# Kernel tuning notes

Hardware: AMD Instinct MI355X
Metric: run time of the kernel (lower is better)

## Reference

```python
import math
import jax, jax.numpy as jnp
import numpy as np

B, L, D, H, DFF, T, V = 512, 128, 128, 4, 256, 2048, 20000
LN_EPS = 1e-5
LOG_SIGMA0 = math.log(0.1)


def _keygen(base):
    c = [0]
    def nk():
        k = jax.random.fold_in(base, c[0]); c[0] += 1
        return k
    return nk


def bayes_linear(x, wmu, wls, bmu, bls, nk):
    # weight = mu + exp(log_sigma) * eps (fresh eps every call, as in BayesLinear.forward)
    w = wmu + jnp.exp(wls) * jax.random.normal(nk(), wmu.shape, wmu.dtype)
    b = bmu + jnp.exp(bls) * jax.random.normal(nk(), bmu.shape, bmu.dtype)
    return jnp.einsum('...d,od->...o', x, w) + b


def layer_norm(x, g, b):
    m = x.mean(-1, keepdims=True)
    v = ((x - m) ** 2).mean(-1, keepdims=True)
    return (x - m) / jnp.sqrt(v + LN_EPS) * g + b


def mha(q, k, v, wmu, wls, bmu, bls, nk):
    # wmu: [4, D, D] for q, k, v, o projections
    dk = D // H
    def proj(x, i):
        return bayes_linear(x, wmu[i], wls[i], bmu[i], bls[i], nk)
    def split(x):
        return x.reshape(B, L, H, dk).transpose(0, 2, 1, 3)
    Q, K, Vh = split(proj(q, 0)), split(proj(k, 1)), split(proj(v, 2))
    probs = jax.nn.softmax(jnp.einsum('bhqd,bhkd->bhqk', Q, K) / math.sqrt(dk), axis=-1)
    out = jnp.einsum('bhqk,bhkd->bhqd', probs, Vh).transpose(0, 2, 1, 3).reshape(B, L, D)
    return bayes_linear(out, wmu[3], wls[3], bmu[3], bls[3], nk)


def setup_inputs() -> dict:
    key = jax.random.key(0)
    ks = iter(jax.random.split(key, 64))
    def u(shape, fan_in):
        s = 1.0 / math.sqrt(fan_in)
        return jax.random.uniform(next(ks), shape, jnp.float32, -s, s)
    def ls(shape):
        return jnp.full(shape, LOG_SIGMA0, jnp.float32)
    return dict(
        event_set=jax.random.randint(next(ks), (B, L), 0, V),
        time=jax.random.uniform(next(ks), (B, L), jnp.float32),
        mask=jax.random.randint(next(ks), (B, L), 0, L),
        set_size=jax.random.randint(next(ks), (B,), 1, L),
        emb=jax.random.normal(next(ks), (V, D), jnp.float32),
        dec_wmu=u((2, 8, D, D), D), dec_wls=ls((2, 8, D, D)),
        dec_bmu=u((2, 8, D), D), dec_bls=ls((2, 8, D)),
        ffn1_wmu=u((2, DFF, D), D), ffn1_wls=ls((2, DFF, D)),
        ffn1_bmu=u((2, DFF), D), ffn1_bls=ls((2, DFF)),
        ffn2_wmu=u((2, D, DFF), DFF), ffn2_wls=ls((2, D, DFF)),
        ffn2_bmu=u((2, D), DFF), ffn2_bls=ls((2, D)),
        ln_g=jnp.ones((2, 3, D), jnp.float32), ln_b=jnp.zeros((2, 3, D), jnp.float32),
        alpha_wmu=u((5, T, D), D), alpha_wls=ls((5, T, D)),
        alpha_bmu=u((5, T), D), alpha_bls=ls((5, T)),
        at_wmu=u((5, 1, D), D), at_wls=ls((5, 1, D)),
        at_bmu=u((5, 1), D), at_bls=ls((5, 1)),
        em_w=u((5, T, D), D), em_b=u((5, T), D),
        es_w=u((5, T, D), D), es_b=u((5, T), D),
        tm_w=u((5, 1, D), D), tm_b=u((5, 1), D),
        ts_w=u((5, 1, D), D), ts_b=u((5, 1), D),
    )


def reference(event_set, time, mask, set_size, emb,
              dec_wmu, dec_wls, dec_bmu, dec_bls,
              ffn1_wmu, ffn1_wls, ffn1_bmu, ffn1_bls,
              ffn2_wmu, ffn2_wls, ffn2_bmu, ffn2_bls,
              ln_g, ln_b, alpha_wmu, alpha_wls, alpha_bmu, alpha_bls,
              at_wmu, at_wls, at_bmu, at_bls,
              em_w, em_b, es_w, es_b, tm_w, tm_b, ts_w, ts_b):
    nk = _keygen(jax.random.key(42))
    x = emb[event_set]                                     # [B, L, D]
    # sinusoidal positional encoding driven by `mask` (integer positions)
    pos = mask.astype(jnp.float32)
    div = jnp.exp(jnp.arange(D, dtype=jnp.float32) * (-math.log(10000.0) / D))
    ang = pos[..., None] * div                             # [B, L, D]
    pos_enc = jnp.where((mask % 2 == 0)[..., None], jnp.sin(ang), jnp.cos(ang))
    inp_x = x + pos_enc
    # two decoder layers: self-attn on x, cross-attn against inp_x (dropout = eval identity)
    for l in range(2):
        a = mha(x, x, x, dec_wmu[l, :4], dec_wls[l, :4], dec_bmu[l, :4], dec_bls[l, :4], nk)
        x = layer_norm(x + a, ln_g[l, 0], ln_b[l, 0])
        a = mha(x, inp_x, inp_x, dec_wmu[l, 4:], dec_wls[l, 4:], dec_bmu[l, 4:], dec_bls[l, 4:], nk)
        x = layer_norm(x + a, ln_g[l, 1], ln_b[l, 1])
        h1 = jax.nn.relu(bayes_linear(x, ffn1_wmu[l], ffn1_wls[l], ffn1_bmu[l], ffn1_bls[l], nk))
        f = bayes_linear(h1, ffn2_wmu[l], ffn2_wls[l], ffn2_bmu[l], ffn2_bls[l], nk)
        x = layer_norm(x + f, ln_g[l, 2], ln_b[l, 2])
    h = x[:, 0, :]                                          # [B, D]
    # 5 Bayesian alpha heads -> softmax over mixture dim (vectorized over k)
    aw = alpha_wmu + jnp.exp(alpha_wls) * jax.random.normal(nk(), alpha_wmu.shape)
    ab = alpha_bmu + jnp.exp(alpha_bls) * jax.random.normal(nk(), alpha_bmu.shape)
    alpha = jax.nn.softmax(jnp.einsum('bd,ktd->btk', h, aw) + ab.T[None], axis=2)   # [B, T, 5]
    atw = at_wmu + jnp.exp(at_wls) * jax.random.normal(nk(), at_wmu.shape)
    atb = at_bmu + jnp.exp(at_bls) * jax.random.normal(nk(), at_bmu.shape)
    alpha_t = jax.nn.softmax(jnp.einsum('bd,kd->bk', h, atw[:, 0]) + atb[:, 0][None], axis=1)  # [B, 5]
    # mixture of 5 reparameterized Gaussian predictors (plain Linears)
    means = jnp.einsum('bd,ktd->bkt', h, em_w) + em_b[None]          # [B, 5, T]
    stds = jnp.exp(jnp.einsum('bd,ktd->bkt', h, es_w) + es_b[None])
    noise_e = jax.random.normal(nk(), (B, 5, T))
    event_pred = jnp.sum(jnp.swapaxes(alpha, 1, 2) * (means + stds * noise_e), axis=1)   # [B, T]
    tmeans = jnp.einsum('bd,kd->bk', h, tm_w[:, 0]) + tm_b[:, 0][None]                   # [B, 5]
    tstds = jnp.exp(jnp.einsum('bd,kd->bk', h, ts_w[:, 0]) + ts_b[:, 0][None])
    noise_t = jax.random.normal(nk(), (B, 5))
    time_pred = jnp.sum(alpha_t * (tmeans + tstds * noise_t), axis=1, keepdims=True)     # [B, 1]
    return event_pred, time_pred
```

## Files before the change

kernel.cpp:

```cpp
#include <hip/hip_runtime.h>
#include <cstdint>
#include <cstddef>


#define NB   512
#define NL   128
#define ND   128
#define NH   4
#define NDFF 256
#define NT   2048
#define BL   (NB * NL)

typedef __attribute__((ext_vector_type(8))) short bf16x8;
typedef __attribute__((ext_vector_type(4))) float f32x4;

__host__ __device__ __forceinline__ void tf2x32(uint32_t k0, uint32_t k1,
                                                uint32_t x0, uint32_t x1,
                                                uint32_t& o0, uint32_t& o1)
{
  const uint32_t ks2 = k0 ^ k1 ^ 0x1BD11BDAu;
  x0 += k0; x1 += k1;
#define TF_RND(r) { x0 += x1; x1 = (x1 << (r)) | (x1 >> (32 - (r))); x1 ^= x0; }
  TF_RND(13) TF_RND(15) TF_RND(26) TF_RND(6)
  x0 += k1;  x1 += ks2 + 1u;
  TF_RND(17) TF_RND(29) TF_RND(16) TF_RND(24)
  x0 += ks2; x1 += k0 + 2u;
  TF_RND(13) TF_RND(15) TF_RND(26) TF_RND(6)
  x0 += k0;  x1 += k1 + 3u;
  TF_RND(17) TF_RND(29) TF_RND(16) TF_RND(24)
  x0 += k1;  x1 += ks2 + 4u;
  TF_RND(13) TF_RND(15) TF_RND(26) TF_RND(6)
  x0 += ks2; x1 += k0 + 5u;
#undef TF_RND
  o0 = x0; o1 = x1;
}

__device__ __forceinline__ float erfinv32(float x)
{
  float w = -log1pf(-__fmul_rn(x, x));
  float p;
  if (w < 5.0f) {
    w = w - 2.5f;
    p = 2.81022636e-08f;
    p = __fadd_rn( 3.43273939e-07f, __fmul_rn(p, w));
    p = __fadd_rn(-3.5233877e-06f,  __fmul_rn(p, w));
    p = __fadd_rn(-4.39150654e-06f, __fmul_rn(p, w));
    p = __fadd_rn( 0.00021858087f,  __fmul_rn(p, w));
// ... 106 lines not shown
    int t = i - SA_F2W; int s = t >> 15;
    mu = f2_wmu + t; ls = f2_wls + t;
    c = 18u + 20u * s; idx = (uint32_t)(t & 32767);
    bf_dst = BW_F2 + t;
  } else if (i < SA_AW) {
    int t = i - SA_F2B; int s = t >> 7;
    mu = f2_bmu + t; ls = f2_bls + t;
    c = 19u + 20u * s; idx = (uint32_t)(t & 127);
    f32_dst = BF_F2B + t;
  } else if (i < SA_AB) {
    int t = i - SA_AW;
    mu = a_wmu + t; ls = a_wls + t; c = 40u; idx = (uint32_t)t;
    bf_dst = BW_AW + t;
  } else if (i < SA_ATW) {
    int t = i - SA_AB;
    mu = a_bmu + t; ls = a_bls + t; c = 41u; idx = (uint32_t)t;
    f32_dst = BF_AB + t;
  } else if (i < SA_ATB) {
    int t = i - SA_ATW;
    mu = at_wmu + t; ls = at_wls + t; c = 42u; idx = (uint32_t)t;
    f32_dst = BF_ATW + t;
  } else {
    int t = i - SA_ATB;
    mu = at_bmu + t; ls = at_bls + t; c = 43u; idx = (uint32_t)t;
    f32_dst = BF_ATB + t;
  }
  uint32_t k0, k1;
  tf2x32(0u, 42u, 0u, c, k0, k1);
  float v = mu[0] + expf(ls[0]) * jax_normal_idx(k0, k1, idx);
  if (bf_dst >= 0) wbf[bf_dst] = f2bf(v);
  else             wf32[f32_dst] = v;
}

__global__ __launch_bounds__(256) void embed_pe_kernel(
    const int* __restrict__ ev, const int* __restrict__ mask,
    const float* __restrict__ emb, float* __restrict__ X,
    ushort* __restrict__ Xbf, ushort* __restrict__ INPXbf)
{
  int i = blockIdx.x * 256 + threadIdx.x;
  if (i >= BL * ND) return;
  int d  = i & (ND - 1);
  int bl = i >> 7;
  int e  = ev[bl];
  int mk = mask[bl];
  float x   = emb[(size_t)e * ND + d];
  float div = expf((float)d * (float)(-9.210340371976184 / 128.0));
  float ang = (float)mk * div;
  float pe  = ((mk & 1) == 0) ? sinf(ang) : cosf(ang);
  X[i]      = x;
  Xbf[i]    = f2bf(x);
  INPXbf[i] = f2bf(x + pe);
}

#define STR 136

template<int CROSS>
__global__ __launch_bounds__(512) void attn_block_kernel(
    const ushort* __restrict__ Xbf, const ushort* __restrict__ KVsrc,
    float* __restrict__ X, ushort* __restrict__ Xout,
    const ushort* __restrict__ W4,
    const float* __restrict__ B4,
    const float* __restrict__ lng, const float* __restrict__ lnb)
{
  __shared__ ushort Wl[128][STR];
  __shared__ ushort Kt[128][STR];
  __shared__ ushort Vt[128][STR];
  __shared__ ushort B0[128][STR];

  const int b = blockIdx.x;
  const int tid = threadIdx.x;
  const int w = tid >> 6, l = tid & 63;
  const int g = l >> 4, r16 = l & 15;
  const size_t abase = (size_t)b * (NL * ND);
  const ushort* Aq  = Xbf + abase;
  const ushort* Akv = (CROSS ? KVsrc : Xbf) + abase;
  const f32x4 zero = {0.f, 0.f, 0.f, 0.f};

  auto stageW = [&](const ushort* src) {
#pragma unroll
    for (int it = 0; it < 4; ++it) {
      int ci = tid + it * 512;
      int row = ci >> 4, q = ci & 15;
      *(bf16x8*)&Wl[row][q * 8] = *(const bf16x8*)(src + (size_t)row * 128 + q * 8);
    }
  };
  auto gemmG = [&](const ushort* A, f32x4 (&acc)[8]) {
#pragma unroll
    for (int c = 0; c < 8; ++c) acc[c] = zero;
#pragma unroll
    for (int ks = 0; ks < 4; ++ks) {
      bf16x8 a = *(const bf16x8*)(A + (size_t)(16 * w + r16) * 128 + 32 * ks + 8 * g);
#pragma unroll
      for (int c = 0; c < 8; ++c) {
        bf16x8 wv = *(const bf16x8*)&Wl[16 * c + r16][32 * ks + 8 * g];
        acc[c] = __builtin_amdgcn_mfma_f32_16x16x32_bf16(a, wv, acc[c], 0, 0, 0);
      }
    }
  };

  f32x4 acc[8];

  stageW(W4 + 0 * 16384);
  __syncthreads();
  gemmG(Aq, acc);
#pragma unroll
  for (int c = 0; c < 8; ++c) {
    float bb = B4[0 * 128 + 16 * c + r16];
#pragma unroll
    for (int r = 0; r < 4; ++r)
      B0[16 * w + 4 * g + r][16 * c + r16] = f2bf(acc[c][r] + bb);
  }
  __syncthreads();

  stageW(W4 + 1 * 16384);
  __syncthreads();
  gemmG(Akv, acc);
#pragma unroll
  for (int c = 0; c < 8; ++c) {
    float bb = B4[1 * 128 + 16 * c + r16];
#pragma unroll
    for (int r = 0; r < 4; ++r)
      Kt[16 * w + 4 * g + r][16 * c + r16] = f2bf(acc[c][r] + bb);
  }
  __syncthreads();

  stageW(W4 + 2 * 16384);
  __syncthreads();
  gemmG(Akv, acc);
#pragma unroll
  for (int c = 0; c < 8; ++c) {
    float bb = B4[2 * 128 + 16 * c + r16];
#pragma unroll
    for (int r = 0; r < 4; ++r)
      Vt[16 * c + r16][16 * w + 4 * g + r] = f2bf(acc[c][r] + bb);
  }
  __syncthreads();

  const float scale = 0.1767766952966369f;
  f32x4 oacc[4][2];
#pragma unroll
  for (int h = 0; h < 4; ++h) { oacc[h][0] = zero; oacc[h][1] = zero; }

#pragma unroll
  for (int h = 0; h < 4; ++h) {
    bf16x8 qa = *(const bf16x8*)&B0[16 * w + r16][32 * h + 8 * g];
    f32x4 s[8];
#pragma unroll
    for (int c = 0; c < 8; ++c) {
      bf16x8 kv = *(const bf16x8*)&Kt[16 * c + r16][32 * h + 8 * g];
      s[c] = __builtin_amdgcn_mfma_f32_16x16x32_bf16(qa, kv, zero, 0, 0, 0);
    }
#pragma unroll
    for (int r = 0; r < 4; ++r) {
      float v[8]; float m = -1e30f;
#pragma unroll
      for (int c = 0; c < 8; ++c) { v[c] = s[c][r] * scale; m = fmaxf(m, v[c]); }
#pragma unroll
      for (int o = 1; o < 16; o <<= 1) m = fmaxf(m, __shfl_xor(m, o));
      float sum = 0.f;
#pragma unroll
      for (int c = 0; c < 8; ++c) { v[c] = __expf(v[c] - m); sum += v[c]; }
#pragma unroll
      for (int o = 1; o < 16; o <<= 1) sum += __shfl_xor(sum, o);
      const float inv = 1.0f / sum;
#pragma unroll
      for (int c = 0; c < 8; ++c)
        Wl[16 * w + 4 * g + r][16 * c + r16] = f2bf(v[c] * inv);
    }
#pragma unroll
    for (int ks = 0; ks < 4; ++ks) {
      bf16x8 pa = *(const bf16x8*)&Wl[16 * w + r16][32 * ks + 8 * g];
#pragma unroll
      for (int cc = 0; cc < 2; ++cc) {
        bf16x8 vv = *(const bf16x8*)&Vt[32 * h + 16 * cc + r16][32 * ks + 8 * g];
        oacc[h][cc] = __builtin_amdgcn_mfma_f32_16x16x32_bf16(pa, vv, oacc[h][cc], 0, 0, 0);
      }
    }
  }

#pragma unroll
  for (int h = 0; h < 4; ++h)
#pragma unroll
    for (int cc = 0; cc < 2; ++cc)
#pragma unroll
      for (int r = 0; r < 4; ++r)
        B0[16 * w + 4 * g + r][32 * h + 16 * cc + r16] = f2bf(oacc[h][cc][r]);
  __syncthreads();

  stageW(W4 + 3 * 16384);
  __syncthreads();
  f32x4 acc2[8];
#pragma unroll
  for (int c = 0; c < 8; ++c) acc2[c] = zero;
#pragma unroll
  for (int ks = 0; ks < 4; ++ks) {
    bf16x8 a = *(const bf16x8*)&B0[16 * w + r16][32 * ks + 8 * g];
#pragma unroll
    for (int c = 0; c < 8; ++c) {
      bf16x8 wv = *(const bf16x8*)&Wl[16 * c + r16][32 * ks + 8 * g];
      acc2[c] = __builtin_amdgcn_mfma_f32_16x16x32_bf16(a, wv, acc2[c], 0, 0, 0);
    }
  }

  float gg[8], lb[8], bo[8];
#pragma unroll
  for (int c = 0; c < 8; ++c) {
    gg[c] = lng[16 * c + r16];
    lb[c] = lnb[16 * c + r16];
    bo[c] = B4[3 * 128 + 16 * c + r16];
  }
#pragma unroll
  for (int r = 0; r < 4; ++r) {
    const int row = 16 * w + 4 * g + r;
    const size_t gr = abase + (size_t)row * ND;
    float xv[8];
#pragma unroll
    for (int c = 0; c < 8; ++c)
      xv[c] = acc2[c][r] + bo[c] + X[gr + 16 * c + r16];
    float s = 0.f;
#pragma unroll
    for (int c = 0; c < 8; ++c) s += xv[c];
#pragma unroll
    for (int o = 1; o < 16; o <<= 1) s += __shfl_xor(s, o);
    const float mean = s * (1.0f / 128.0f);
    float q = 0.f;
#pragma unroll
    for (int c = 0; c < 8; ++c) { float d = xv[c] - mean; q += d * d; }
#pragma unroll
    for (int o = 1; o < 16; o <<= 1) q += __shfl_xor(q, o);
    const float inv = 1.0f / sqrtf(q * (1.0f / 128.0f) + 1e-5f);
#pragma unroll
    for (int c = 0; c < 8; ++c) {
      float o = (xv[c] - mean) * inv * gg[c] + lb[c];
      X[gr + 16 * c + r16] = o;
      Xout[gr + 16 * c + r16] = f2bf(o);
    }
  }
}

__global__ __launch_bounds__(512) void ffn_block_kernel(
    const ushort* __restrict__ Xbf, float* __restrict__ X, ushort* __restrict__ Xout,
    const ushort* __restrict__ W1, const float* __restrict__ B1,
    const ushort* __restrict__ W2, const float* __restrict__ B2,
    const float* __restrict__ lng, const float* __restrict__ lnb,
    ushort* __restrict__ Hb)
{
  __shared__ ushort Wa[128][STR];
  __shared__ ushort Wb[128][STR];
  __shared__ ushort Ha[128][STR];
  __shared__ ushort Hc[128][STR];

  const int b = blockIdx.x;
  const int tid = threadIdx.x;
  const int w = tid >> 6, l = tid & 63;
  const int g = l >> 4, r16 = l & 15;
  const size_t abase = (size_t)b * (NL * ND);
  const ushort* A = Xbf + abase;
  const f32x4 zero = {0.f, 0.f, 0.f, 0.f};

#pragma unroll
  for (int it = 0; it < 8; ++it) {
    int ci = tid + it * 512;
    int row = ci >> 4, q = ci & 15;
    bf16x8 v = *(const bf16x8*)(W1 + (size_t)row * 128 + q * 8);
    if (row < 128) *(bf16x8*)&Wa[row][q * 8] = v;
    else           *(bf16x8*)&Wb[row - 128][q * 8] = v;
  }
  __syncthreads();

  f32x4 acc1[16];
#pragma unroll
  for (int c = 0; c < 16; ++c) acc1[c] = zero;
#pragma unroll
  for (int ks = 0; ks < 4; ++ks) {
    bf16x8 a = *(const bf16x8*)(A + (size_t)(16 * w + r16) * 128 + 32 * ks + 8 * g);
#pragma unroll
    for (int c = 0; c < 16; ++c) {
      bf16x8 wv = (c < 8)
        ? *(const bf16x8*)&Wa[16 * c + r16][32 * ks + 8 * g]
        : *(const bf16x8*)&Wb[16 * (c - 8) + r16][32 * ks + 8 * g];
      acc1[c] = __builtin_amdgcn_mfma_f32_16x16x32_bf16(a, wv, acc1[c], 0, 0, 0);
    }
  }
#pragma unroll
  for (int c = 0; c < 16; ++c) {
    float bb = B1[16 * c + r16];
#pragma unroll
    for (int r = 0; r < 4; ++r) {
      float o = fmaxf(acc1[c][r] + bb, 0.f);
      if (c < 8) Ha[16 * w + 4 * g + r][16 * c + r16] = f2bf(o);
      else       Hc[16 * w + 4 * g + r][16 * (c - 8) + r16] = f2bf(o);
    }
  }
  __syncthreads();

#pragma unroll
  for (int it = 0; it < 8; ++it) {
    int ci = tid + it * 512;
    int row = ci >> 5, q = ci & 31;
    bf16x8 v = *(const bf16x8*)(W2 + (size_t)row * 256 + q * 8);
    if (q < 16) *(bf16x8*)&Wa[row][q * 8] = v;
    else        *(bf16x8*)&Wb[row][(q - 16) * 8] = v;
  }
  __syncthreads();

  f32x4 acc2[8];
#pragma unroll
  for (int c = 0; c < 8; ++c) acc2[c] = zero;
#pragma unroll
  for (int ks = 0; ks < 8; ++ks) {
    bf16x8 a = (ks < 4)
      ? *(const bf16x8*)&Ha[16 * w + r16][32 * ks + 8 * g]
      : *(const bf16x8*)&Hc[16 * w + r16][32 * (ks - 4) + 8 * g];
#pragma unroll
    for (int c = 0; c < 8; ++c) {
      bf16x8 wv = (ks < 4)
        ? *(const bf16x8*)&Wa[16 * c + r16][32 * ks + 8 * g]
        : *(const bf16x8*)&Wb[16 * c + r16][32 * (ks - 4) + 8 * g];
      acc2[c] = __builtin_amdgcn_mfma_f32_16x16x32_bf16(a, wv, acc2[c], 0, 0, 0);
    }
  }

  float gg[8], lb[8], bo[8];
#pragma unroll
  for (int c = 0; c < 8; ++c) {
    gg[c] = lng[16 * c + r16];
    lb[c] = lnb[16 * c + r16];
    bo[c] = B2[16 * c + r16];
  }
#pragma unroll
  for (int r = 0; r < 4; ++r) {
    const int row = 16 * w + 4 * g + r;
    const size_t gr = abase + (size_t)row * ND;
    float xv[8];
#pragma unroll
    for (int c = 0; c < 8; ++c)
      xv[c] = acc2[c][r] + bo[c] + X[gr + 16 * c + r16];
    float s = 0.f;
#pragma unroll
    for (int c = 0; c < 8; ++c) s += xv[c];
#pragma unroll
    for (int o = 1; o < 16; o <<= 1) s += __shfl_xor(s, o);
    const float mean = s * (1.0f / 128.0f);
    float q = 0.f;
#pragma unroll
    for (int c = 0; c < 8; ++c) { float d = xv[c] - mean; q += d * d; }
#pragma unroll
    for (int o = 1; o < 16; o <<= 1) q += __shfl_xor(q, o);
    const float inv = 1.0f / sqrtf(q * (1.0f / 128.0f) + 1e-5f);
#pragma unroll
    for (int c = 0; c < 8; ++c) {
      float o = (xv[c] - mean) * inv * gg[c] + lb[c];
      X[gr + 16 * c + r16] = o;
      Xout[gr + 16 * c + r16] = f2bf(o);
      if (Hb && row == 0)
        Hb[(size_t)b * ND + 16 * c + r16] = f2bf(o);
    }
  }
}

template<int WFP32>
__global__ __launch_bounds__(256) void head_gemm(
    const ushort* __restrict__ A,
    const ushort* __restrict__ Wb16, const float* __restrict__ Wf32,
    const float* __restrict__ bias, float* __restrict__ C, int ldc)
{
  __shared__ char smem[128 * 132 * 4];
  ushort (*Wl)[STR] = (ushort(*)[STR])smem;
  float  (*Cl)[132] = (float(*)[132])smem;

  const int tid = threadIdx.x;
  const int bn = blockIdx.x * 128;
  const int bm = blockIdx.y * 128;
  const int w = tid >> 6, l = tid & 63;
  const int r16 = l & 15, g = l >> 4;
  const f32x4 zero = {0.f, 0.f, 0.f, 0.f};

#pragma unroll
  for (int it = 0; it < 8; ++it) {
    int ci = tid + it * 256;
    int row = ci >> 4, q = ci & 15;
    if (WFP32) {
      float4 v0 = *(const float4*)(Wf32 + (size_t)(bn + row) * 128 + q * 8);
      float4 v1 = *(const float4*)(Wf32 + (size_t)(bn + row) * 128 + q * 8 + 4);
      bf16x8 o;
      o[0] = f2bf(v0.x); o[1] = f2bf(v0.y); o[2] = f2bf(v0.z); o[3] = f2bf(v0.w);
      o[4] = f2bf(v1.x); o[5] = f2bf(v1.y); o[6] = f2bf(v1.z); o[7] = f2bf(v1.w);
      *(bf16x8*)&Wl[row][q * 8] = o;
    } else {
      *(bf16x8*)&Wl[row][q * 8] =
          *(const bf16x8*)(Wb16 + (size_t)(bn + row) * 128 + q * 8);
    }
  }
  __syncthreads();

  f32x4 acc[2][8];
#pragma unroll
  for (int t = 0; t < 2; ++t)
#pragma unroll
    for (int c = 0; c < 8; ++c) acc[t][c] = zero;
#pragma unroll
  for (int ks = 0; ks < 4; ++ks) {
    bf16x8 a[2];
#pragma unroll
    for (int t = 0; t < 2; ++t)
      a[t] = *(const bf16x8*)(A + (size_t)(bm + 32 * w + 16 * t + r16) * 128
                              + 32 * ks + 8 * g);
    bf16x8 wv[8];
#pragma unroll
    for (int c = 0; c < 8; ++c)
      wv[c] = *(const bf16x8*)&Wl[16 * c + r16][32 * ks + 8 * g];
#pragma unroll
    for (int t = 0; t < 2; ++t)
#pragma unroll
      for (int c = 0; c < 8; ++c)
        acc[t][c] = __builtin_amdgcn_mfma_f32_16x16x32_bf16(a[t], wv[c], acc[t][c], 0, 0, 0);
  }

  float bcol[8];
#pragma unroll
  for (int c = 0; c < 8; ++c) bcol[c] = bias[bn + 16 * c + r16];
  __syncthreads();

#pragma unroll
  for (int t = 0; t < 2; ++t)
#pragma unroll
    for (int c = 0; c < 8; ++c)
#pragma unroll
      for (int r = 0; r < 4; ++r)
        Cl[32 * w + 16 * t + 4 * g + r][16 * c + r16] = acc[t][c][r] + bcol[c];
  __syncthreads();
#pragma unroll
  for (int i = 0; i < 16; ++i) {
    int ci = l + 64 * i;
    int row = 32 * w + (ci >> 5), q = ci & 31;
    float4 v = *(const float4*)&Cl[row][4 * q];
    *(float4*)(C + (size_t)(bm + row) * ldc + bn + 4 * q) = v;
  }
}

__global__ __launch_bounds__(256) void event_head_kernel(
    const float* __restrict__ LA, const float* __restrict__ MB,
    const float* __restrict__ SB, float* __restrict__ out,
    uint32_t k0, uint32_t k1)
{
  int i = blockIdx.x * 256 + threadIdx.x;
  if (i >= NB * NT) return;
  int b = i >> 11, t = i & (NT - 1);
  size_t base = (size_t)b * (5 * NT) + t;
  float lg[5];
  float mx = -1e30f;
#pragma unroll
  for (int k = 0; k < 5; ++k) { lg[k] = LA[base + (size_t)k * NT]; mx = fmaxf(mx, lg[k]); }
  float se = 0.f;
#pragma unroll
  for (int k = 0; k < 5; ++k) { lg[k] = expf(lg[k] - mx); se += lg[k]; }
  float inv = 1.0f / se;
  float acc = 0.f;
#pragma unroll
  for (int k = 0; k < 5; ++k) {
    float nz = jax_normal_idx(k0, k1, (uint32_t)((b * 5 + k) * NT + t));
    float mean = MB[base + (size_t)k * NT];
    float sd   = expf(SB[base + (size_t)k * NT]);
    acc += (lg[k] * inv) * (mean + sd * nz);
  }
  out[i] = acc;
}

__global__ __launch_bounds__(64) void time_head_kernel(
    const float* __restrict__ X, const float* __restrict__ atw,
    const float* __restrict__ atb, const float* __restrict__ tmw,
    const float* __restrict__ tmb, const float* __restrict__ tsw,
    const float* __restrict__ tsb, float* __restrict__ out,
    uint32_t k0, uint32_t k1)
{
  const int b = blockIdx.x;
  const int l = threadIdx.x;
  const float* h = X + (size_t)b * (NL * ND);
  const float h0 = h[l], h1 = h[l + 64];
  float lg[5], tm[5], tsl[5];
#pragma unroll
  for (int k = 0; k < 5; ++k) {
    float s0 = fmaf(h0, atw[k * ND + l], h1 * atw[k * ND + l + 64]);
    float s1 = fmaf(h0, tmw[k * ND + l], h1 * tmw[k * ND + l + 64]);
    float s2 = fmaf(h0, tsw[k * ND + l], h1 * tsw[k * ND + l + 64]);
#pragma unroll
    for (int o = 32; o; o >>= 1) {
      s0 += __shfl_xor(s0, o);
      s1 += __shfl_xor(s1, o);
      s2 += __shfl_xor(s2, o);
    }
    lg[k] = s0 + atb[k]; tm[k] = s1 + tmb[k]; tsl[k] = s2 + tsb[k];
  }
  if (l == 0) {
    float mx = lg[0];
    for (int k = 1; k < 5; ++k) mx = fmaxf(mx, lg[k]);
    float se = 0.f;
    for (int k = 0; k < 5; ++k) { lg[k] = expf(lg[k] - mx); se += lg[k]; }
    float acc = 0.f;
    for (int k = 0; k < 5; ++k) {
      float nz = jax_normal_idx(k0, k1, (uint32_t)(b * 5 + k));
      acc += (lg[k] / se) * (tm[k] + expf(tsl[k]) * nz);
    }
    out[b] = acc;
  }
}

extern "C" void kernel_launch(void* const* d_in, const int* in_sizes, int n_in,
                              void* d_out, int out_size, void* d_ws, size_t ws_size,
                              hipStream_t stream)
{
// ... 4 lines not shown
  const float* emb     = (const float*)d_in[4];
  const float* dec_wmu = (const float*)d_in[5];
  const float* dec_wls = (const float*)d_in[6];
  const float* dec_bmu = (const float*)d_in[7];
  const float* dec_bls = (const float*)d_in[8];
  const float* f1_wmu  = (const float*)d_in[9];
  const float* f1_wls  = (const float*)d_in[10];
  const float* f1_bmu  = (const float*)d_in[11];
  const float* f1_bls  = (const float*)d_in[12];
  const float* f2_wmu  = (const float*)d_in[13];
  const float* f2_wls  = (const float*)d_in[14];
  const float* f2_bmu  = (const float*)d_in[15];
  const float* f2_bls  = (const float*)d_in[16];
  const float* ln_g    = (const float*)d_in[17];
  const float* ln_b    = (const float*)d_in[18];
  const float* a_wmu   = (const float*)d_in[19];
  const float* a_wls   = (const float*)d_in[20];
  const float* a_bmu   = (const float*)d_in[21];
  const float* a_bls   = (const float*)d_in[22];
  const float* at_wmu  = (const float*)d_in[23];
  const float* at_wls  = (const float*)d_in[24];
  const float* at_bmu  = (const float*)d_in[25];
  const float* at_bls  = (const float*)d_in[26];
  const float* em_w    = (const float*)d_in[27];
  const float* em_b    = (const float*)d_in[28];
  const float* es_w    = (const float*)d_in[29];
  const float* es_b    = (const float*)d_in[30];
  const float* tm_w    = (const float*)d_in[31];
  const float* tm_b    = (const float*)d_in[32];
  const float* ts_w    = (const float*)d_in[33];
  const float* ts_b    = (const float*)d_in[34];

  float* ws = (float*)d_ws;
  const size_t SZ = (size_t)BL * ND;
  const size_t HN = (size_t)NB * 5 * NT;
  float*  X      = ws;
  ushort* Xbf    = (ushort*)(ws + SZ);
  ushort* INPXbf = (ushort*)(ws + SZ) + SZ;
  float*  LA     = ws + 2 * SZ;
  float*  MBo    = LA + HN;
  float*  SBo    = MBo + HN;
  ushort* WBF    = (ushort*)(SBo + HN);
  float*  WF32   = SBo + HN + BW_TOT / 2;
  ushort* Hbuf   = (ushort*)(WF32 + BF_TOT + 3);

  uint32_t fk0[46], fk1[46];
  for (uint32_t c = 0; c < 46; ++c) tf2x32(0u, 42u, 0u, c, fk0[c], fk1[c]);

  sample_all_kernel<<<dim3((SA_TOT + 255) / 256), dim3(256), 0, stream>>>(
      dec_wmu, dec_wls, dec_bmu, dec_bls,
      f1_wmu, f1_wls, f1_bmu, f1_bls,
      f2_wmu, f2_wls, f2_bmu, f2_bls,
      a_wmu, a_wls, a_bmu, a_bls,
      at_wmu, at_wls, at_bmu, at_bls, WBF, WF32);

  embed_pe_kernel<<<dim3((BL * ND) / 256), dim3(256), 0, stream>>>(
      ev, mask, emb, X, Xbf, INPXbf);

  for (int l = 0; l < 2; ++l) {
    const int s_self = l * 8, s_cross = l * 8 + 4;
    attn_block_kernel<0><<<dim3(NB), dim3(512), 0, stream>>>(
        Xbf, nullptr, X, Xbf,
        WBF + BW_DEC + (size_t)s_self * 16384,
        WF32 + BF_DECB + (size_t)s_self * 128,
        ln_g + (size_t)(l * 3 + 0) * ND, ln_b + (size_t)(l * 3 + 0) * ND);
    attn_block_kernel<1><<<dim3(NB), dim3(512), 0, stream>>>(
        Xbf, INPXbf, X, Xbf,
        WBF + BW_DEC + (size_t)s_cross * 16384,
        WF32 + BF_DECB + (size_t)s_cross * 128,
        ln_g + (size_t)(l * 3 + 1) * ND, ln_b + (size_t)(l * 3 + 1) * ND);
    ffn_block_kernel<<<dim3(NB), dim3(512), 0, stream>>>(
        Xbf, X, Xbf,
        WBF + BW_F1 + (size_t)l * 32768, WF32 + BF_F1B + (size_t)l * 256,
        WBF + BW_F2 + (size_t)l * 32768, WF32 + BF_F2B + (size_t)l * 128,
        ln_g + (size_t)(l * 3 + 2) * ND, ln_b + (size_t)(l * 3 + 2) * ND,
        (l == 1) ? Hbuf : nullptr);
  }

  head_gemm<0><<<dim3(80, 4), dim3(256), 0, stream>>>(
      Hbuf, WBF + BW_AW, nullptr, WF32 + BF_AB, LA, 5 * NT);
  head_gemm<1><<<dim3(80, 4), dim3(256), 0, stream>>>(
      Hbuf, nullptr, em_w, em_b, MBo, 5 * NT);
  head_gemm<1><<<dim3(80, 4), dim3(256), 0, stream>>>(
      Hbuf, nullptr, es_w, es_b, SBo, 5 * NT);

  float* out = (float*)d_out;
  event_head_kernel<<<dim3((NB * NT) / 256), dim3(256), 0, stream>>>(
      LA, MBo, SBo, out, fk0[44], fk1[44]);
  time_head_kernel<<<dim3(NB), dim3(64), 0, stream>>>(
      X, WF32 + BF_ATW, WF32 + BF_ATB, tm_w, tm_b, ts_w, ts_b,
      out + (size_t)NB * NT, fk0[45], fk1[45]);
}
```

Measured before the change: 353.0 us.

## Fuse embedding and all six decoder sublayers into one persistent per-batch kernel

Replaces the embedding kernel and six separate attention/FFN block launches with one mega-kernel per batch element. The residual stream lives in registers (fp32) and LDS (bf16) across all sublayers, and the positional-encoded cross-attention input is computed in registers. This removes the global round trips of the fp32 X, its bf16 copy and the encoder input between kernels, plus launch overhead. In exchange it uses more registers and LDS (launch bounds 512,2), and it shrinks the probability staging buffer by writing it in chunks, which may add LDS traffic and cost occupancy.

```diff
diff --git a/kernel.cpp b/kernel.cpp
--- a/kernel.cpp
+++ b/kernel.cpp
@@ -13,6 +13,8 @@
 
 typedef __attribute__((ext_vector_type(8))) short bf16x8;
 typedef __attribute__((ext_vector_type(4))) float f32x4;
+
+#define MFMA16(a, b, c) __builtin_amdgcn_mfma_f32_16x16x32_bf16((a), (b), (c), 0, 0, 0)
 
 __host__ __device__ __forceinline__ void tf2x32(uint32_t k0, uint32_t k1,
                                                 uint32_t x0, uint32_t x1,
@@ -185,329 +187,326 @@
   else             wf32[f32_dst] = v;
 }
 
-__global__ __launch_bounds__(256) void embed_pe_kernel(
+#define STR 136
+
+__global__ __launch_bounds__(512, 2) void decoder_mega_kernel(
     const int* __restrict__ ev, const int* __restrict__ mask,
-    const float* __restrict__ emb, float* __restrict__ X,
-    ushort* __restrict__ Xbf, ushort* __restrict__ INPXbf)
-{
-  int i = blockIdx.x * 256 + threadIdx.x;
-  if (i >= BL * ND) return;
-  int d  = i & (ND - 1);
-  int bl = i >> 7;
-  int e  = ev[bl];
-  int mk = mask[bl];
-  float x   = emb[(size_t)e * ND + d];
-  float div = expf((float)d * (float)(-9.210340371976184 / 128.0));
-  float ang = (float)mk * div;
-  float pe  = ((mk & 1) == 0) ? sinf(ang) : cosf(ang);
-  X[i]      = x;
-  Xbf[i]    = f2bf(x);
-  INPXbf[i] = f2bf(x + pe);
-}
-
-#define STR 136
-
-template<int CROSS>
-__global__ __launch_bounds__(512) void attn_block_kernel(
-    const ushort* __restrict__ Xbf, const ushort* __restrict__ KVsrc,
-    float* __restrict__ X, ushort* __restrict__ Xout,
-    const ushort* __restrict__ W4,
-    const float* __restrict__ B4,
-    const float* __restrict__ lng, const float* __restrict__ lnb)
-{
-  __shared__ ushort Wl[128][STR];
+    const float* __restrict__ emb,
+    const ushort* __restrict__ WBF, const float* __restrict__ WF32,
+    const float* __restrict__ lng_all, const float* __restrict__ lnb_all,
+    float* __restrict__ Xh, ushort* __restrict__ Hb)
+{
+  __shared__ ushort WL[128][STR];
   __shared__ ushort Kt[128][STR];
   __shared__ ushort Vt[128][STR];
-  __shared__ ushort B0[128][STR];
+  __shared__ ushort Xb[128][STR];
+  __shared__ ushort Ps[128][72];
 
   const int b = blockIdx.x;
   const int tid = threadIdx.x;
   const int w = tid >> 6, l = tid & 63;
   const int g = l >> 4, r16 = l & 15;
-  const size_t abase = (size_t)b * (NL * ND);
-  const ushort* Aq  = Xbf + abase;
-  const ushort* Akv = (CROSS ? KVsrc : Xbf) + abase;
   const f32x4 zero = {0.f, 0.f, 0.f, 0.f};
 
-  auto stageW = [&](const ushort* src) {
+  auto stageS = [&](ushort (*dst)[STR], const ushort* src, int srcStride) {
 #pragma unroll
     for (int it = 0; it < 4; ++it) {
       int ci = tid + it * 512;
       int row = ci >> 4, q = ci & 15;
-      *(bf16x8*)&Wl[row][q * 8] = *(const bf16x8*)(src + (size_t)row * 128 + q * 8);
+      *(bf16x8*)&dst[row][q * 8] = *(const bf16x8*)(src + (size_t)row * srcStride + q * 8);
     }
   };
-  auto gemmG = [&](const ushort* A, f32x4 (&acc)[8]) {
-#pragma unroll
-    for (int c = 0; c < 8; ++c) acc[c] = zero;
+
+  float xreg[8][4];
+  {
+    int ecr[4];
+#pragma unroll
+    for (int r = 0; r < 4; ++r) ecr[r] = ev[b * NL + 16 * w + 4 * g + r];
+#pragma unroll
+    for (int c = 0; c < 8; ++c)
+#pragma unroll
+      for (int r = 0; r < 4; ++r) {
+        float x = emb[(size_t)ecr[r] * ND + 16 * c + r16];
+        xreg[c][r] = x;
+        Xb[16 * w + 4 * g + r][16 * c + r16] = f2bf(x);
+      }
+  }
+  bf16x8 inpx[4];
+  {
+    const int row = 16 * w + r16;
+    const int ea = ev[b * NL + row];
+    const int mk = mask[b * NL + row];
+    const bool even = (mk & 1) == 0;
+    const float fm = (float)mk;
 #pragma unroll
     for (int ks = 0; ks < 4; ++ks) {
-      bf16x8 a = *(const bf16x8*)(A + (size_t)(16 * w + r16) * 128 + 32 * ks + 8 * g);
+      float4 x0 = *(const float4*)(emb + (size_t)ea * ND + 32 * ks + 8 * g);
+      float4 x1 = *(const float4*)(emb + (size_t)ea * ND + 32 * ks + 8 * g + 4);
+      float xs[8] = {x0.x, x0.y, x0.z, x0.w, x1.x, x1.y, x1.z, x1.w};
+      bf16x8 v;
+#pragma unroll
+      for (int e = 0; e < 8; ++e) {
+        int d = 32 * ks + 8 * g + e;
+        float div = expf((float)d * (float)(-9.210340371976184 / 128.0));
+        float ang = fm * div;
+        float pe = even ? sinf(ang) : cosf(ang);
+        v[e] = (short)f2bf(xs[e] + pe);
+      }
+      inpx[ks] = v;
+    }
+  }
+
+#pragma unroll 1
+  for (int st = 0; st < 6; ++st) {
+    const int lay = st / 3, m = st - 3 * lay;
+    const float* lng = lng_all + (size_t)(lay * 3 + m) * ND;
+    const float* lnb = lnb_all + (size_t)(lay * 3 + m) * ND;
+    f32x4 acc2[8];
+#pragma unroll
+    for (int c = 0; c < 8; ++c) acc2[c] = zero;
+    float bo[8];
+
+    __syncthreads();
+    if (m < 2) {
+      const int s0 = lay * 8 + m * 4;
+      const ushort* W4 = WBF + BW_DEC + (size_t)s0 * 16384;
+      const float*  B4 = WF32 + BF_DECB + (size_t)s0 * 128;
+
+      stageS(WL, W4, 128);
+      __syncthreads();
+      f32x4 qacc[8];
+#pragma unroll
+      for (int c = 0; c < 8; ++c) qacc[c] = zero;
+#pragma unroll
+      for (int ks = 0; ks < 4; ++ks) {
+        bf16x8 a = *(const bf16x8*)&Xb[16 * w + r16][32 * ks + 8 * g];
+#pragma unroll
+        for (int c = 0; c < 8; ++c) {
+          bf16x8 wv = *(const bf16x8*)&WL[16 * c + r16][32 * ks + 8 * g];
+          qacc[c] = MFMA16(a, wv, qacc[c]);
+        }
+      }
+      __syncthreads();
+      stageS(WL, W4 + 16384, 128);
+      __syncthreads();
+      {
+        f32x4 kacc[8];
+#pragma unroll
+        for (int c = 0; c < 8; ++c) kacc[c] = zero;
+#pragma unroll
+        for (int ks = 0; ks < 4; ++ks) {
+          bf16x8 a = (m == 0) ? *(const bf16x8*)&Xb[16 * w + r16][32 * ks + 8 * g]
+                              : inpx[ks];
+#pragma unroll
+          for (int c = 0; c < 8; ++c) {
+            bf16x8 wv = *(const bf16x8*)&WL[16 * c + r16][32 * ks + 8 * g];
+            kacc[c] = MFMA16(a, wv, kacc[c]);
+          }
+        }
+#pragma unroll
+        for (int c = 0; c < 8; ++c) {
+          float kb = B4[128 + 16 * c + r16];
+#pragma unroll
+          for (int r = 0; r < 4; ++r)
+            Kt[16 * w + 4 * g + r][16 * c + r16] = f2bf(kacc[c][r] + kb);
+        }
+      }
+      __syncthreads();
+      stageS(WL, W4 + 2 * 16384, 128);
+      __syncthreads();
+      {
+        f32x4 vacc[8];
+#pragma unroll
+        for (int c = 0; c < 8; ++c) vacc[c] = zero;
+#pragma unroll
+        for (int ks = 0; ks < 4; ++ks) {
+          bf16x8 a = (m == 0) ? *(const bf16x8*)&Xb[16 * w + r16][32 * ks + 8 * g]
+                              : inpx[ks];
+#pragma unroll
+          for (int c = 0; c < 8; ++c) {
+            bf16x8 wv = *(const bf16x8*)&WL[16 * c + r16][32 * ks + 8 * g];
+            vacc[c] = MFMA16(a, wv, vacc[c]);
+          }
+        }
+#pragma unroll
+        for (int c = 0; c < 8; ++c) {
+          float vb = B4[256 + 16 * c + r16];
+#pragma unroll
+          for (int r = 0; r < 4; ++r)
+            Vt[16 * c + r16][16 * w + 4 * g + r] = f2bf(vacc[c][r] + vb);
+        }
+      }
+      __syncthreads();
 #pragma unroll
       for (int c = 0; c < 8; ++c) {
-        bf16x8 wv = *(const bf16x8*)&Wl[16 * c + r16][32 * ks + 8 * g];
-        acc[c] = __builtin_amdgcn_mfma_f32_16x16x32_bf16(a, wv, acc[c], 0, 0, 0);
-      }
+        float qb = B4[16 * c + r16];
+#pragma unroll
+        for (int r = 0; r < 4; ++r)
+          WL[16 * w + 4 * g + r][16 * c + r16] = f2bf(qacc[c][r] + qb);
+      }
+      __syncthreads();
+
+      const float scale = 0.1767766952966369f;
+      f32x4 oacc[4][2];
+#pragma unroll
+      for (int h = 0; h < 4; ++h) { oacc[h][0] = zero; oacc[h][1] = zero; }
+#pragma unroll 1
+      for (int h = 0; h < 4; ++h) {
+        bf16x8 qa = *(const bf16x8*)&WL[16 * w + r16][32 * h + 8 * g];
+        f32x4 s[8];
+#pragma unroll
+        for (int c = 0; c < 8; ++c) {
+          bf16x8 kv = *(const bf16x8*)&Kt[16 * c + r16][32 * h + 8 * g];
+          s[c] = MFMA16(qa, kv, zero);
+        }
+        float pv[4][8];
+#pragma unroll
+        for (int r = 0; r < 4; ++r) {
+          float v[8]; float mx = -1e30f;
+#pragma unroll
+          for (int c = 0; c < 8; ++c) { v[c] = s[c][r] * scale; mx = fmaxf(mx, v[c]); }
+#pragma unroll
+          for (int o = 1; o < 16; o <<= 1) mx = fmaxf(mx, __shfl_xor(mx, o));
+          float sum = 0.f;
+#pragma unroll
+          for (int c = 0; c < 8; ++c) { v[c] = __expf(v[c] - mx); sum += v[c]; }
+#pragma unroll
+          for (int o = 1; o < 16; o <<= 1) sum += __shfl_xor(sum, o);
+          float inv = 1.0f / sum;
+#pragma unroll
+          for (int c = 0; c < 8; ++c) pv[r][c] = v[c] * inv;
+        }
+#pragma unroll
+        for (int kc = 0; kc < 4; ++kc) {
+          const int po = (kc & 1) * 32;
+#pragma unroll
+          for (int c2 = 0; c2 < 2; ++c2)
+#pragma unroll
+            for (int r = 0; r < 4; ++r)
+              Ps[16 * w + 4 * g + r][po + 16 * c2 + r16] = f2bf(pv[r][2 * kc + c2]);
+          bf16x8 pa = *(const bf16x8*)&Ps[16 * w + r16][po + 8 * g];
+#pragma unroll
+          for (int cc = 0; cc < 2; ++cc) {
+            bf16x8 vv = *(const bf16x8*)&Vt[32 * h + 16 * cc + r16][32 * kc + 8 * g];
+            oacc[h][cc] = MFMA16(pa, vv, oacc[h][cc]);
+          }
+        }
+      }
+      __syncthreads();
+#pragma unroll
+      for (int h = 0; h < 4; ++h)
+#pragma unroll
+        for (int cc = 0; cc < 2; ++cc)
+#pragma unroll
+          for (int r = 0; r < 4; ++r)
+            Kt[16 * w + 4 * g + r][32 * h + 16 * cc + r16] = f2bf(oacc[h][cc][r]);
+      stageS(WL, W4 + 3 * 16384, 128);
+      __syncthreads();
+#pragma unroll
+      for (int ks = 0; ks < 4; ++ks) {
+        bf16x8 a = *(const bf16x8*)&Kt[16 * w + r16][32 * ks + 8 * g];
+#pragma unroll
+        for (int c = 0; c < 8; ++c) {
+          bf16x8 wv = *(const bf16x8*)&WL[16 * c + r16][32 * ks + 8 * g];
+          acc2[c] = MFMA16(a, wv, acc2[c]);
+        }
+      }
+#pragma unroll
+      for (int c = 0; c < 8; ++c) bo[c] = B4[384 + 16 * c + r16];
+    } else {
+      const ushort* W1 = WBF + BW_F1 + (size_t)lay * 32768;
+      const ushort* W2 = WBF + BW_F2 + (size_t)lay * 32768;
+      const float*  B1 = WF32 + BF_F1B + (size_t)lay * 256;
+      const float*  B2 = WF32 + BF_F2B + (size_t)lay * 128;
+      stageS(WL, W1, 128);
+      stageS(Kt, W1 + (size_t)128 * 128, 128);
+      __syncthreads();
+      f32x4 acc1[16];
+#pragma unroll
+      for (int c = 0; c < 16; ++c) acc1[c] = zero;
+#pragma unroll
+      for (int ks = 0; ks < 4; ++ks) {
+        bf16x8 a = *(const bf16x8*)&Xb[16 * w + r16][32 * ks + 8 * g];
+#pragma unroll
+        for (int c = 0; c < 8; ++c) {
+          bf16x8 w1v = *(const bf16x8*)&WL[16 * c + r16][32 * ks + 8 * g];
+          acc1[c] = MFMA16(a, w1v, acc1[c]);
+          bf16x8 w2v = *(const bf16x8*)&Kt[16 * c + r16][32 * ks + 8 * g];
+          acc1[8 + c] = MFMA16(a, w2v, acc1[8 + c]);
+        }
+      }
+      __syncthreads();
+#pragma unroll
+      for (int c = 0; c < 16; ++c) {
+        float bb = B1[16 * c + r16];
+#pragma unroll
+        for (int r = 0; r < 4; ++r) {
+          float o = fmaxf(acc1[c][r] + bb, 0.f);
+          if (c < 8) WL[16 * w + 4 * g + r][16 * c + r16] = f2bf(o);
+          else       Kt[16 * w + 4 * g + r][16 * (c - 8) + r16] = f2bf(o);
+        }
+      }
+      stageS(Vt, W2, 256);
+      __syncthreads();
+#pragma unroll
+      for (int ks = 0; ks < 4; ++ks) {
+        bf16x8 a = *(const bf16x8*)&WL[16 * w + r16][32 * ks + 8 * g];
+#pragma unroll
+        for (int c = 0; c < 8; ++c) {
+          bf16x8 wv = *(const bf16x8*)&Vt[16 * c + r16][32 * ks + 8 * g];
+          acc2[c] = MFMA16(a, wv, acc2[c]);
+        }
+      }
+      __syncthreads();
+      stageS(Vt, W2 + 128, 256);
+      __syncthreads();
+#pragma unroll
+      for (int ks = 0; ks < 4; ++ks) {
+        bf16x8 a = *(const bf16x8*)&Kt[16 * w + r16][32 * ks + 8 * g];
+#pragma unroll
+        for (int c = 0; c < 8; ++c) {
+          bf16x8 wv = *(const bf16x8*)&Vt[16 * c + r16][32 * ks + 8 * g];
+          acc2[c] = MFMA16(a, wv, acc2[c]);
+        }
+      }
+#pragma unroll
+      for (int c = 0; c < 8; ++c) bo[c] = B2[16 * c + r16];
     }
-  };
-
-  f32x4 acc[8];
-
-  stageW(W4 + 0 * 16384);
-  __syncthreads();
-  gemmG(Aq, acc);
-#pragma unroll
-  for (int c = 0; c < 8; ++c) {
-    float bb = B4[0 * 128 + 16 * c + r16];
-#pragma unroll
-    for (int r = 0; r < 4; ++r)
-      B0[16 * w + 4 * g + r][16 * c + r16] = f2bf(acc[c][r] + bb);
-  }
-  __syncthreads();
-
-  stageW(W4 + 1 * 16384);
-  __syncthreads();
-  gemmG(Akv, acc);
-#pragma unroll
-  for (int c = 0; c < 8; ++c) {
-    float bb = B4[1 * 128 + 16 * c + r16];
-#pragma unroll
-    for (int r = 0; r < 4; ++r)
-      Kt[16 * w + 4 * g + r][16 * c + r16] = f2bf(acc[c][r] + bb);
-  }
-  __syncthreads();
-
-  stageW(W4 + 2 * 16384);
-  __syncthreads();
-  gemmG(Akv, acc);
-#pragma unroll
-  for (int c = 0; c < 8; ++c) {
-    float bb = B4[2 * 128 + 16 * c + r16];
-#pragma unroll
-    for (int r = 0; r < 4; ++r)
-      Vt[16 * c + r16][16 * w + 4 * g + r] = f2bf(acc[c][r] + bb);
-  }
-  __syncthreads();
-
-  const float scale = 0.1767766952966369f;
-  f32x4 oacc[4][2];
-#pragma unroll
-  for (int h = 0; h < 4; ++h) { oacc[h][0] = zero; oacc[h][1] = zero; }
-
-#pragma unroll
-  for (int h = 0; h < 4; ++h) {
-    bf16x8 qa = *(const bf16x8*)&B0[16 * w + r16][32 * h + 8 * g];
-    f32x4 s[8];
+
+    float gg[8], lb[8];
+#pragma unroll
+    for (int c = 0; c < 8; ++c) { gg[c] = lng[16 * c + r16]; lb[c] = lnb[16 * c + r16]; }
+#pragma unroll
+    for (int r = 0; r < 4; ++r) {
+      float xv[8];
+#pragma unroll
+      for (int c = 0; c < 8; ++c) xv[c] = acc2[c][r] + bo[c] + xreg[c][r];
+      float s = 0.f;
+#pragma unroll
+      for (int c = 0; c < 8; ++c) s += xv[c];
+#pragma unroll
+      for (int o = 1; o < 16; o <<= 1) s += __shfl_xor(s, o);
+      float mean = s * (1.0f / 128.0f);
+      float q = 0.f;
+#pragma unroll
+      for (int c = 0; c < 8; ++c) { float d = xv[c] - mean; q += d * d; }
+#pragma unroll
+      for (int o = 1; o < 16; o <<= 1) q += __shfl_xor(q, o);
+      float inv = 1.0f / sqrtf(q * (1.0f / 128.0f) + 1e-5f);
+#pragma unroll
+      for (int c = 0; c < 8; ++c) {
+        float o = (xv[c] - mean) * inv * gg[c] + lb[c];
+        xreg[c][r] = o;
+        Xb[16 * w + 4 * g + r][16 * c + r16] = f2bf(o);
+      }
+    }
+  }
+
+  if (w == 0 && g == 0) {
 #pragma unroll
     for (int c = 0; c < 8; ++c) {
-      bf16x8 kv = *(const bf16x8*)&Kt[16 * c + r16][32 * h + 8 * g];
-      s[c] = __builtin_amdgcn_mfma_f32_16x16x32_bf16(qa, kv, zero, 0, 0, 0);
-    }
-#pragma unroll
-    for (int r = 0; r < 4; ++r) {
-      float v[8]; float m = -1e30f;
-#pragma unroll
-      for (int c = 0; c < 8; ++c) { v[c] = s[c][r] * scale; m = fmaxf(m, v[c]); }
-#pragma unroll
-      for (int o = 1; o < 16; o <<= 1) m = fmaxf(m, __shfl_xor(m, o));
-      float sum = 0.f;
-#pragma unroll
-      for (int c = 0; c < 8; ++c) { v[c] = __expf(v[c] - m); sum += v[c]; }
-#pragma unroll
-      for (int o = 1; o < 16; o <<= 1) sum += __shfl_xor(sum, o);
-      const float inv = 1.0f / sum;
-#pragma unroll
-      for (int c = 0; c < 8; ++c)
-        Wl[16 * w + 4 * g + r][16 * c + r16] = f2bf(v[c] * inv);
-    }
-#pragma unroll
-    for (int ks = 0; ks < 4; ++ks) {
-      bf16x8 pa = *(const bf16x8*)&Wl[16 * w + r16][32 * ks + 8 * g];
-#pragma unroll
-      for (int cc = 0; cc < 2; ++cc) {
-        bf16x8 vv = *(const bf16x8*)&Vt[32 * h + 16 * cc + r16][32 * ks + 8 * g];
-        oacc[h][cc] = __builtin_amdgcn_mfma_f32_16x16x32_bf16(pa, vv, oacc[h][cc], 0, 0, 0);
-      }
-    }
-  }
-
-#pragma unroll
-  for (int h = 0; h < 4; ++h)
-#pragma unroll
-    for (int cc = 0; cc < 2; ++cc)
-#pragma unroll
-      for (int r = 0; r < 4; ++r)
-        B0[16 * w + 4 * g + r][32 * h + 16 * cc + r16] = f2bf(oacc[h][cc][r]);
-  __syncthreads();
-
-  stageW(W4 + 3 * 16384);
-  __syncthreads();
-  f32x4 acc2[8];
-#pragma unroll
-  for (int c = 0; c < 8; ++c) acc2[c] = zero;
-#pragma unroll
-  for (int ks = 0; ks < 4; ++ks) {
-    bf16x8 a = *(const bf16x8*)&B0[16 * w + r16][32 * ks + 8 * g];
-#pragma unroll
-    for (int c = 0; c < 8; ++c) {
-      bf16x8 wv = *(const bf16x8*)&Wl[16 * c + r16][32 * ks + 8 * g];
-      acc2[c] = __builtin_amdgcn_mfma_f32_16x16x32_bf16(a, wv, acc2[c], 0, 0, 0);
-    }
-  }
-
-  float gg[8], lb[8], bo[8];
-#pragma unroll
-  for (int c = 0; c < 8; ++c) {
-    gg[c] = lng[16 * c + r16];
-    lb[c] = lnb[16 * c + r16];
-    bo[c] = B4[3 * 128 + 16 * c + r16];
-  }
-#pragma unroll
-  for (int r = 0; r < 4; ++r) {
-    const int row = 16 * w + 4 * g + r;
-    const size_t gr = abase + (size_t)row * ND;
-    float xv[8];
-#pragma unroll
-    for (int c = 0; c < 8; ++c)
-      xv[c] = acc2[c][r] + bo[c] + X[gr + 16 * c + r16];
-    float s = 0.f;
-#pragma unroll
-    for (int c = 0; c < 8; ++c) s += xv[c];
-#pragma unroll
-    for (int o = 1; o < 16; o <<= 1) s += __shfl_xor(s, o);
-    const float mean = s * (1.0f / 128.0f);
-    float q = 0.f;
-#pragma unroll
-    for (int c = 0; c < 8; ++c) { float d = xv[c] - mean; q += d * d; }
-#pragma unroll
-    for (int o = 1; o < 16; o <<= 1) q += __shfl_xor(q, o);
-    const float inv = 1.0f / sqrtf(q * (1.0f / 128.0f) + 1e-5f);
-#pragma unroll
-    for (int c = 0; c < 8; ++c) {
-      float o = (xv[c] - mean) * inv * gg[c] + lb[c];
-      X[gr + 16 * c + r16] = o;
-      Xout[gr + 16 * c + r16] = f2bf(o);
-    }
-  }
-}
-
-__global__ __launch_bounds__(512) void ffn_block_kernel(
-    const ushort* __restrict__ Xbf, float* __restrict__ X, ushort* __restrict__ Xout,
-    const ushort* __restrict__ W1, const float* __restrict__ B1,
-    const ushort* __restrict__ W2, const float* __restrict__ B2,
-    const float* __restrict__ lng, const float* __restrict__ lnb,
-    ushort* __restrict__ Hb)
-{
-  __shared__ ushort Wa[128][STR];
-  __shared__ ushort Wb[128][STR];
-  __shared__ ushort Ha[128][STR];
-  __shared__ ushort Hc[128][STR];
-
-  const int b = blockIdx.x;
-  const int tid = threadIdx.x;
-  const int w = tid >> 6, l = tid & 63;
-  const int g = l >> 4, r16 = l & 15;
-  const size_t abase = (size_t)b * (NL * ND);
-  const ushort* A = Xbf + abase;
-  const f32x4 zero = {0.f, 0.f, 0.f, 0.f};
-
-#pragma unroll
-  for (int it = 0; it < 8; ++it) {
-    int ci = tid + it * 512;
-    int row = ci >> 4, q = ci & 15;
-    bf16x8 v = *(const bf16x8*)(W1 + (size_t)row * 128 + q * 8);
-    if (row < 128) *(bf16x8*)&Wa[row][q * 8] = v;
-    else           *(bf16x8*)&Wb[row - 128][q * 8] = v;
-  }
-  __syncthreads();
-
-  f32x4 acc1[16];
-#pragma unroll
-  for (int c = 0; c < 16; ++c) acc1[c] = zero;
-#pragma unroll
-  for (int ks = 0; ks < 4; ++ks) {
-    bf16x8 a = *(const bf16x8*)(A + (size_t)(16 * w + r16) * 128 + 32 * ks + 8 * g);
-#pragma unroll
-    for (int c = 0; c < 16; ++c) {
-      bf16x8 wv = (c < 8)
-        ? *(const bf16x8*)&Wa[16 * c + r16][32 * ks + 8 * g]
-        : *(const bf16x8*)&Wb[16 * (c - 8) + r16][32 * ks + 8 * g];
-      acc1[c] = __builtin_amdgcn_mfma_f32_16x16x32_bf16(a, wv, acc1[c], 0, 0, 0);
-    }
-  }
-#pragma unroll
-  for (int c = 0; c < 16; ++c) {
-    float bb = B1[16 * c + r16];
-#pragma unroll
-    for (int r = 0; r < 4; ++r) {
-      float o = fmaxf(acc1[c][r] + bb, 0.f);
-      if (c < 8) Ha[16 * w + 4 * g + r][16 * c + r16] = f2bf(o);
-      else       Hc[16 * w + 4 * g + r][16 * (c - 8) + r16] = f2bf(o);
-    }
-  }
-  __syncthreads();
-
-#pragma unroll
-  for (int it = 0; it < 8; ++it) {
-    int ci = tid + it * 512;
-    int row = ci >> 5, q = ci & 31;
-    bf16x8 v = *(const bf16x8*)(W2 + (size_t)row * 256 + q * 8);
-    if (q < 16) *(bf16x8*)&Wa[row][q * 8] = v;
-    else        *(bf16x8*)&Wb[row][(q - 16) * 8] = v;
-  }
-  __syncthreads();
-
-  f32x4 acc2[8];
-#pragma unroll
-  for (int c = 0; c < 8; ++c) acc2[c] = zero;
-#pragma unroll
-  for (int ks = 0; ks < 8; ++ks) {
-    bf16x8 a = (ks < 4)
-      ? *(const bf16x8*)&Ha[16 * w + r16][32 * ks + 8 * g]
-      : *(const bf16x8*)&Hc[16 * w + r16][32 * (ks - 4) + 8 * g];
-#pragma unroll
-    for (int c = 0; c < 8; ++c) {
-      bf16x8 wv = (ks < 4)
-        ? *(const bf16x8*)&Wa[16 * c + r16][32 * ks + 8 * g]
-        : *(const bf16x8*)&Wb[16 * c + r16][32 * (ks - 4) + 8 * g];
-      acc2[c] = __builtin_amdgcn_mfma_f32_16x16x32_bf16(a, wv, acc2[c], 0, 0, 0);
-    }
-  }
-
-  float gg[8], lb[8], bo[8];
-#pragma unroll
-  for (int c = 0; c < 8; ++c) {
-    gg[c] = lng[16 * c + r16];
-    lb[c] = lnb[16 * c + r16];
-    bo[c] = B2[16 * c + r16];
-  }
-#pragma unroll
-  for (int r = 0; r < 4; ++r) {
-    const int row = 16 * w + 4 * g + r;
-    const size_t gr = abase + (size_t)row * ND;
-    float xv[8];
-#pragma unroll
-    for (int c = 0; c < 8; ++c)
-      xv[c] = acc2[c][r] + bo[c] + X[gr + 16 * c + r16];
-    float s = 0.f;
-#pragma unroll
-    for (int c = 0; c < 8; ++c) s += xv[c];
-#pragma unroll
-    for (int o = 1; o < 16; o <<= 1) s += __shfl_xor(s, o);
-    const float mean = s * (1.0f / 128.0f);
-    float q = 0.f;
-#pragma unroll
-    for (int c = 0; c < 8; ++c) { float d = xv[c] - mean; q += d * d; }
-#pragma unroll
-    for (int o = 1; o < 16; o <<= 1) q += __shfl_xor(q, o);
-    const float inv = 1.0f / sqrtf(q * (1.0f / 128.0f) + 1e-5f);
-#pragma unroll
-    for (int c = 0; c < 8; ++c) {
-      float o = (xv[c] - mean) * inv * gg[c] + lb[c];
-      X[gr + 16 * c + r16] = o;
-      Xout[gr + 16 * c + r16] = f2bf(o);
-      if (Hb && row == 0)
-        Hb[(size_t)b * ND + 16 * c + r16] = f2bf(o);
+      Xh[(size_t)b * ND + 16 * c + r16] = xreg[c][0];
+      Hb[(size_t)b * ND + 16 * c + r16] = f2bf(xreg[c][0]);
     }
   }
 }
@@ -567,7 +566,7 @@
     for (int t = 0; t < 2; ++t)
 #pragma unroll
       for (int c = 0; c < 8; ++c)
-        acc[t][c] = __builtin_amdgcn_mfma_f32_16x16x32_bf16(a[t], wv[c], acc[t][c], 0, 0, 0);
+        acc[t][c] = MFMA16(a[t], wv[c], acc[t][c]);
   }
 
   float bcol[8];
@@ -621,7 +620,7 @@
 }
 
 __global__ __launch_bounds__(64) void time_head_kernel(
-    const float* __restrict__ X, const float* __restrict__ atw,
+    const float* __restrict__ Xh, const float* __restrict__ atw,
     const float* __restrict__ atb, const float* __restrict__ tmw,
     const float* __restrict__ tmb, const float* __restrict__ tsw,
     const float* __restrict__ tsb, float* __restrict__ out,
@@ -629,7 +628,7 @@
 {
   const int b = blockIdx.x;
   const int l = threadIdx.x;
-  const float* h = X + (size_t)b * (NL * ND);
+  const float* h = Xh + (size_t)b * ND;
   const float h0 = h[l], h1 = h[l + 64];
   float lg[5], tm[5], tsl[5];
 #pragma unroll
@@ -700,17 +699,14 @@
   const float* ts_b    = (const float*)d_in[34];
 
   float* ws = (float*)d_ws;
-  const size_t SZ = (size_t)BL * ND;
   const size_t HN = (size_t)NB * 5 * NT;
-  float*  X      = ws;
-  ushort* Xbf    = (ushort*)(ws + SZ);
-  ushort* INPXbf = (ushort*)(ws + SZ) + SZ;
-  float*  LA     = ws + 2 * SZ;
-  float*  MBo    = LA + HN;
-  float*  SBo    = MBo + HN;
-  ushort* WBF    = (ushort*)(SBo + HN);
-  float*  WF32   = SBo + HN + BW_TOT / 2;
-  ushort* Hbuf   = (ushort*)(WF32 + BF_TOT + 3);
+  float*  LA   = ws;
+  float*  MBo  = LA + HN;
+  float*  SBo  = MBo + HN;
+  ushort* WBF  = (ushort*)(SBo + HN);
+  float*  WF32 = SBo + HN + BW_TOT / 2;
+  ushort* Hb   = (ushort*)(WF32 + BF_TOT + 3);
+  float*  Xh   = (float*)(Hb + (size_t)NB * ND);
 
   uint32_t fk0[46], fk1[46];
   for (uint32_t c = 0; c < 46; ++c) tf2x32(0u, 42u, 0u, c, fk0[c], fk1[c]);
@@ -722,40 +718,20 @@
       a_wmu, a_wls, a_bmu, a_bls,
       at_wmu, at_wls, at_bmu, at_bls, WBF, WF32);
 
-  embed_pe_kernel<<<dim3((BL * ND) / 256), dim3(256), 0, stream>>>(
-      ev, mask, emb, X, Xbf, INPXbf);
-
-  for (int l = 0; l < 2; ++l) {
-    const int s_self = l * 8, s_cross = l * 8 + 4;
-    attn_block_kernel<0><<<dim3(NB), dim3(512), 0, stream>>>(
-        Xbf, nullptr, X, Xbf,
-        WBF + BW_DEC + (size_t)s_self * 16384,
-        WF32 + BF_DECB + (size_t)s_self * 128,
-        ln_g + (size_t)(l * 3 + 0) * ND, ln_b + (size_t)(l * 3 + 0) * ND);
-    attn_block_kernel<1><<<dim3(NB), dim3(512), 0, stream>>>(
-        Xbf, INPXbf, X, Xbf,
-        WBF + BW_DEC + (size_t)s_cross * 16384,
-        WF32 + BF_DECB + (size_t)s_cross * 128,
-        ln_g + (size_t)(l * 3 + 1) * ND, ln_b + (size_t)(l * 3 + 1) * ND);
-    ffn_block_kernel<<<dim3(NB), dim3(512), 0, stream>>>(
-        Xbf, X, Xbf,
-        WBF + BW_F1 + (size_t)l * 32768, WF32 + BF_F1B + (size_t)l * 256,
-        WBF + BW_F2 + (size_t)l * 32768, WF32 + BF_F2B + (size_t)l * 128,
-        ln_g + (size_t)(l * 3 + 2) * ND, ln_b + (size_t)(l * 3 + 2) * ND,
-        (l == 1) ? Hbuf : nullptr);
-  }
+  decoder_mega_kernel<<<dim3(NB), dim3(512), 0, stream>>>(
+      ev, mask, emb, WBF, WF32, ln_g, ln_b, Xh, Hb);
 
   head_gemm<0><<<dim3(80, 4), dim3(256), 0, stream>>>(
-      Hbuf, WBF + BW_AW, nullptr, WF32 + BF_AB, LA, 5 * NT);
+      Hb, WBF + BW_AW, nullptr, WF32 + BF_AB, LA, 5 * NT);
   head_gemm<1><<<dim3(80, 4), dim3(256), 0, stream>>>(
-      Hbuf, nullptr, em_w, em_b, MBo, 5 * NT);
+      Hb, nullptr, em_w, em_b, MBo, 5 * NT);
   head_gemm<1><<<dim3(80, 4), dim3(256), 0, stream>>>(
-      Hbuf, nullptr, es_w, es_b, SBo, 5 * NT);
+      Hb, nullptr, es_w, es_b, SBo, 5 * NT);
 
   float* out = (float*)d_out;
   event_head_kernel<<<dim3((NB * NT) / 256), dim3(256), 0, stream>>>(
       LA, MBo, SBo, out, fk0[44], fk1[44]);
   time_head_kernel<<<dim3(NB), dim3(64), 0, stream>>>(
-      X, WF32 + BF_ATW, WF32 + BF_ATB, tm_w, tm_b, ts_w, ts_b,
+      Xh, WF32 + BF_ATW, WF32 + BF_ATB, tm_w, tm_b, ts_w, ts_b,
       out + (size_t)NB * NT, fk0[45], fk1[45]);
 }
```

After: 309.6 us. 1.14x faster.
